# Performance work log

Measured on AMD Instinct MI355X. Metric: run time of the kernel, lower is better.

## Reference

```python
import jax, jax.numpy as jnp
import numpy as np
from jax import lax

B, N, C_IN, C_OUT = 8, 8192, 64, 128
NUM_SAMPLES, K = 2048, 32
EPS = 1e-5


def _bn(x, g, b, m, v):
    # inference-mode BatchNorm1d over channel axis 1; x: [G, C, L]
    scale = g / jnp.sqrt(v + EPS)
    return (x - m[None, :, None]) * scale[None, :, None] + b[None, :, None]


def _conv1x1(x, w):
    # kernel_size=1 Conv1d (no bias); x: [G, Cin, L], w: [Cout, Cin]
    return jnp.einsum('gck,oc->gok', x, w)


def _res_block(x, w1, g1, b1, m1, v1, w2, g2, b2, m2, v2):
    # conv-bn-relu -> conv-bn, residual add, relu (residual_factor=1.0)
    y = jax.nn.relu(_bn(_conv1x1(x, w1), g1, b1, m1, v1))
    y = _bn(_conv1x1(y, w2), g2, b2, m2, v2)
    return jax.nn.relu(y + x)


def _fps(xyz, num_samples):
    # farthest point sampling; xyz: [B,N,3] -> indices [B,S]
    b, n, _ = xyz.shape

    def step(carry, _):
        dists, last_idx = carry
        last_pt = jnp.take_along_axis(xyz, last_idx[:, None, None], axis=1)  # [B,1,3]
        d = jnp.sum((xyz - last_pt) ** 2, axis=-1)  # [B,N]
        dists = jnp.minimum(dists, d)
        nxt = jnp.argmax(dists, axis=-1).astype(jnp.int32)
        return (dists, nxt), last_idx

    init = (jnp.full((b, n), 1e10, xyz.dtype), jnp.zeros((b,), jnp.int32))
    _, idxs = lax.scan(step, init, None, length=num_samples)
    return jnp.transpose(idxs)  # [B,S]


def setup_inputs():
    key = jax.random.key(0)
    ks = jax.random.split(key, 40)
    xyz = jax.random.uniform(ks[0], (B, N, 3), jnp.float32)
    feat = jax.random.normal(ks[1], (B, N, C_IN), jnp.float32)

    def conv_w(k, o, c):
        return jax.random.normal(k, (o, c), jnp.float32) * (1.0 / np.sqrt(c).astype(np.float32))

    def bn_params(k, c):
        k1, k2, k3, k4 = jax.random.split(k, 4)
        return (1.0 + 0.1 * jax.random.normal(k1, (c,), jnp.float32),
                0.1 * jax.random.normal(k2, (c,), jnp.float32),
                0.1 * jax.random.normal(k3, (c,), jnp.float32),
                jax.random.uniform(k4, (c,), jnp.float32, 0.5, 1.5))

    inp = {'xyz': xyz, 'feat': feat}
    inp['te_w'] = conv_w(ks[2], C_OUT, 2 * C_IN)
    inp['te_g'], inp['te_b'], inp['te_m'], inp['te_v'] = bn_params(ks[3], C_OUT)
    for name, base in (('pre', 4), ('pos', 14)):
        inp[name + '_w1'] = jnp.stack([conv_w(ks[base + i], C_OUT, C_OUT) for i in range(2)])
        inp[name + '_w2'] = jnp.stack([conv_w(ks[base + 2 + i], C_OUT, C_OUT) for i in range(2)])
        bn1 = [bn_params(ks[base + 4 + i], C_OUT) for i in range(2)]
        bn2 = [bn_params(ks[base + 6 + i], C_OUT) for i in range(2)]
        for j, s in enumerate(('g', 'b', 'm', 'v')):
            inp[f'{name}_{s}1'] = jnp.stack([bn1[i][j] for i in range(2)])
            inp[f'{name}_{s}2'] = jnp.stack([bn2[i][j] for i in range(2)])
    return inp


def reference(xyz, feat, te_w, te_g, te_b, te_m, te_v,
              pre_w1, pre_w2, pre_g1, pre_b1, pre_m1, pre_v1, pre_g2, pre_b2, pre_m2, pre_v2,
              pos_w1, pos_w2, pos_g1, pos_b1, pos_m1, pos_v1, pos_g2, pos_b2, pos_m2, pos_v2):
    bsz = xyz.shape[0]
    # --- LocalGrouper: FPS centers + kNN grouping + concat center feat ---
    fps_idx = _fps(xyz, NUM_SAMPLES)                                    # [B,S]
    new_xyz = jnp.take_along_axis(xyz, fps_idx[..., None], axis=1)      # [B,S,3]
    ctr_feat = jnp.take_along_axis(feat, fps_idx[..., None], axis=1)    # [B,S,C]
    d2 = jnp.sum((new_xyz[:, :, None, :] - xyz[:, None, :, :]) ** 2, axis=-1)  # [B,S,N]
    _, knn_idx = lax.top_k(-d2, K)                                      # [B,S,K]
    grouped = feat[jnp.arange(bsz)[:, None, None], knn_idx]             # [B,S,K,C]
    ctr = jnp.broadcast_to(ctr_feat[:, :, None, :], grouped.shape)
    nf = jnp.concatenate([grouped, ctr], axis=-1)                       # [B,S,K,2C]
    # --- permute/view -> [B*S, 2C, K] ---
    x = nf.transpose(0, 1, 3, 2).reshape(bsz * NUM_SAMPLES, 2 * C_IN, K)
    x = jax.nn.relu(_bn(_conv1x1(x, te_w), te_g, te_b, te_m, te_v))     # [G,OUT,K]
    for i in range(2):
        x = _res_block(x, pre_w1[i], pre_g1[i], pre_b1[i], pre_m1[i], pre_v1[i],
                       pre_w2[i], pre_g2[i], pre_b2[i], pre_m2[i], pre_v2[i])
    x = jnp.max(x, axis=-1)                                             # adaptive_max_pool1d(.,1)
    x = x.reshape(bsz, NUM_SAMPLES, C_OUT).transpose(0, 2, 1)           # [B,OUT,S]
    for i in range(2):
        x = _res_block(x, pos_w1[i], pos_g1[i], pos_b1[i], pos_m1[i], pos_v1[i],
                       pos_w2[i], pos_g2[i], pos_b2[i], pos_m2[i], pos_v2[i])
    return new_xyz, x
```

## Files before the change

### kernel.cpp

```cpp
#include <hip/hip_runtime.h>

typedef unsigned short u16;
typedef unsigned int   u32;
typedef unsigned long long u64;

#define B_    8
#define N_    8192
#define CIN   64
#define COUT  128
#define NS    2048
#define K_    32
#define LDSPAD 136

typedef __attribute__((ext_vector_type(8))) short short8;
typedef __attribute__((ext_vector_type(4))) float f32x4;
typedef __attribute__((ext_vector_type(2))) float f32x2;

#define MFMA16(a,b,c) __builtin_amdgcn_mfma_f32_16x16x32_bf16(a,b,c,0,0,0)

__device__ __forceinline__ u16 f2bf(float f){
  u32 u = __float_as_uint(f);
  return (u16)((u + 0x7FFFu + ((u >> 16) & 1u)) >> 16);
}
__device__ __forceinline__ float bf2f(u16 h){ u32 u = ((u32)h) << 16; return __uint_as_float(u); }
__device__ __forceinline__ u32 pack2bf(float lo, float hi){ return (u32)f2bf(lo) | ((u32)f2bf(hi) << 16); }

__global__ void wcvt_kernel(const float* __restrict__ s, u16* __restrict__ d, int n){
  int i = blockIdx.x * 256 + threadIdx.x;
  if (i < n) d[i] = f2bf(s[i]);
}

__global__ void clear_kernel(int* __restrict__ fps_idx, u32* __restrict__ done){
  int i = blockIdx.x * 256 + threadIdx.x;
  if (i < B_*NS){ fps_idx[i] = -1; done[i] = 0u; }
}

struct BnPtrs { const float* g[9]; const float* b[9]; const float* m[9]; const float* v[9]; };

__global__ void bn_pre_kernel(BnPtrs p, float* __restrict__ bns){
  int set = blockIdx.x, c = threadIdx.x;
  float sc = p.g[set][c] / sqrtf(p.v[set][c] + 1e-5f);
  bns[set*256 + c]       = sc;
  bns[set*256 + 128 + c] = p.b[set][c] - p.m[set][c] * sc;
}

struct ShFps {
  __align__(16) u64  keyA[2][8];
  __align__(16) f32x4 cA[2][8];
};
struct ShMid {
  __align__(16) u16 X[8][32*LDSPAD];
  __align__(16) float scr[8][128];
};
struct ShPos {
  __align__(16) u16 X[8][32*LDSPAD];
};
union ShAll { ShFps f; ShMid m; ShPos p; char pad[83968]; };

__device__ __forceinline__ void lds_barrier(){
  __builtin_amdgcn_sched_barrier(0);
  asm volatile("s_waitcnt lgkmcnt(0)\n\ts_barrier" ::: "memory");
  __builtin_amdgcn_sched_barrier(0);
}

#define DPP_UMAX(x, ctrl) { \
  u32 o = (u32)__builtin_amdgcn_update_dpp((int)(x), (int)(x), ctrl, 0xf, 0xf, false); \
  x = (o > x) ? o : x; }

__device__ __forceinline__ u32 wave_umax63(u32 x){
  DPP_UMAX(x, 0x111)
  DPP_UMAX(x, 0x112)
  DPP_UMAX(x, 0x114)
  DPP_UMAX(x, 0x118)
  DPP_UMAX(x, 0x142)
  DPP_UMAX(x, 0x143)
  return (u32)__builtin_amdgcn_readlane((int)x, 63);
}

#define FPS_PAIR(m) { \
  f32x2 dx = PXr##m - lx2; \
  f32x2 dy = PYr##m - ly2; \
  f32x2 dz = PZr##m - lz2; \
  f32x2 t0 = dx*dx; \
  f32x2 t1 = dy*dy; \
  f32x2 t2 = dz*dz; \
  f32x2 dd = (t0 + t1) + t2; \
  f32x2 nd; \
  nd.x = fminf(Dr##m.x, dd.x); \
  nd.y = fminf(Dr##m.y, dd.y); \
  Dr##m = nd; \
  fmA = fmaxf(fmA, nd.x); \
  fmB = fmaxf(fmB, nd.y); }

#define FPS_SELK(m) { \
  if (Dr##m.y == wmf){ kk = 2*m + 1; wx = PXr##m.y; wy = PYr##m.y; wz = PZr##m.y; } \
  if (Dr##m.x == wmf){ kk = 2*m;     wx = PXr##m.x; wy = PYr##m.x; wz = PZr##m.x; } }

__device__ __forceinline__ void selmax(u64& ka, f32x4& ca, u64 kb, f32x4 cb){
  bool c = kb > ka;
  ka = c ? kb : ka;
  ca = c ? cb : ca;
}

__device__ void fps_path(const float* __restrict__ xyz, int* __restrict__ fps_idx,
                         ShFps& S, int b, int t){
  #pragma clang fp contract(off)
  const int lane = t & 63, wv = t >> 6;
  const float* xb = xyz + (size_t)b * N_ * 3;
  const int base = t * 16;
  f32x4 raw0, raw1, raw2, raw3, raw4, raw5, raw6, raw7, raw8, raw9, rawA, rawB;
  {
    const f32x4* xv = (const f32x4*)(xb + (size_t)base * 3);
    raw0 = xv[0]; raw1 = xv[1]; raw2 = xv[2];  raw3 = xv[3];
    raw4 = xv[4]; raw5 = xv[5]; raw6 = xv[6];  raw7 = xv[7];
    raw8 = xv[8]; raw9 = xv[9]; rawA = xv[10]; rawB = xv[11];
  }
  f32x2 PXr0,PXr1,PXr2,PXr3,PXr4,PXr5,PXr6,PXr7;
  f32x2 PYr0,PYr1,PYr2,PYr3,PYr4,PYr5,PYr6,PYr7;
  f32x2 PZr0,PZr1,PZr2,PZr3,PZr4,PZr5,PZr6,PZr7;
  #define GETF(k) (k<4?raw0[(k)&3]:k<8?raw1[(k)&3]:k<12?raw2[(k)&3]:k<16?raw3[(k)&3]: \
                   k<20?raw4[(k)&3]:k<24?raw5[(k)&3]:k<28?raw6[(k)&3]:k<32?raw7[(k)&3]: \
                   k<36?raw8[(k)&3]:k<40?raw9[(k)&3]:k<44?rawA[(k)&3]:rawB[(k)&3])
  #define SETP(m) { \
    PXr##m.x = GETF(6*m+0); PXr##m.y = GETF(6*m+3); \
    PYr##m.x = GETF(6*m+1); PYr##m.y = GETF(6*m+4); \
    PZr##m.x = GETF(6*m+2); PZr##m.y = GETF(6*m+5); }
  SETP(0) SETP(1) SETP(2) SETP(3) SETP(4) SETP(5) SETP(6) SETP(7)
  #undef SETP
  #undef GETF
  if (t == 0)
    __hip_atomic_store(fps_idx + b*NS, 0, __ATOMIC_RELAXED, __HIP_MEMORY_SCOPE_AGENT);
  f32x2 Dr0,Dr1,Dr2,Dr3,Dr4,Dr5,Dr6,Dr7;
  Dr0=Dr1=Dr2=Dr3=Dr4=Dr5=Dr6=Dr7=(f32x2){1e10f,1e10f};
  const float sx = xb[0], sy = xb[1], sz = xb[2];
  f32x2 lx2 = {sx,sx}, ly2 = {sy,sy}, lz2 = {sz,sz};
  int my_pi = 0;
  for (int s = 0; s < NS - 1; ++s){
    float fmA = 0.f, fmB = 0.f;
    FPS_PAIR(0) FPS_PAIR(1) FPS_PAIR(2) FPS_PAIR(3)
    FPS_PAIR(4) FPS_PAIR(5) FPS_PAIR(6) FPS_PAIR(7)
    const float fm = fmaxf(fmA, fmB);
    const u32 tbm = __float_as_uint(fm);
    const u32 wmax = wave_umax63(tbm);
    const u64 mask = __ballot(tbm == wmax);
    const int fl = __ffsll((long long)mask) - 1;
    const int sl = s & 1;
    if (lane == fl){
      const float wmf = __uint_as_float(wmax);
      int kk = 0;
      float wx = PXr0.x, wy = PYr0.x, wz = PZr0.x;
      FPS_SELK(7) FPS_SELK(6) FPS_SELK(5) FPS_SELK(4)
      FPS_SELK(3) FPS_SELK(2) FPS_SELK(1) FPS_SELK(0)
      const int pi = base + kk;
      S.keyA[sl][wv] = ((u64)wmax << 13) | (u64)(8191 - pi);
      f32x4 c; c[0] = wx; c[1] = wy; c[2] = wz; c[3] = 0.f;
      S.cA[sl][wv] = c;
    }
    lds_barrier();
    u64 k0 = S.keyA[sl][0], k1 = S.keyA[sl][1], k2 = S.keyA[sl][2], k3 = S.keyA[sl][3];
    u64 k4 = S.keyA[sl][4], k5 = S.keyA[sl][5], k6 = S.keyA[sl][6], k7 = S.keyA[sl][7];
    f32x4 c0 = S.cA[sl][0], c1 = S.cA[sl][1], c2 = S.cA[sl][2], c3 = S.cA[sl][3];
    f32x4 c4 = S.cA[sl][4], c5 = S.cA[sl][5], c6 = S.cA[sl][6], c7 = S.cA[sl][7];
    selmax(k0,c0,k1,c1); selmax(k2,c2,k3,c3); selmax(k4,c4,k5,c5); selmax(k6,c6,k7,c7);
    selmax(k0,c0,k2,c2); selmax(k4,c4,k6,c6);
    selmax(k0,c0,k4,c4);
    lx2.x = c0[0]; lx2.y = c0[0];
    ly2.x = c0[1]; ly2.y = c0[1];
    lz2.x = c0[2]; lz2.y = c0[2];
    const int pi_out = 8191 - (int)(k0 & 0x1FFFull);
    if (lane == (s & 15)) my_pi = pi_out;
    if ((s & 15) == 15 && t < 16)
      __hip_atomic_store(fps_idx + b*NS + s - 14 + t, my_pi,
                         __ATOMIC_RELAXED, __HIP_MEMORY_SCOPE_AGENT);
  }
  if (t < 15)
    __hip_atomic_store(fps_idx + b*NS + (NS - 15) + t, my_pi,
                       __ATOMIC_RELAXED, __HIP_MEMORY_SCOPE_AGENT);
}

__device__ __forceinline__ void zero_acc(f32x4 acc[8][2]){
  #pragma unroll
  for (int mt = 0; mt < 8; ++mt)
    #pragma unroll
    for (int nt = 0; nt < 2; ++nt){
      acc[mt][nt][0] = 0.f; acc[mt][nt][1] = 0.f; acc[mt][nt][2] = 0.f; acc[mt][nt][3] = 0.f;
    }
}

__device__ __forceinline__ void conv_step(const u16* __restrict__ W, const u16* __restrict__ Xw,
                                          int q, int l15, f32x4 acc[8][2]){
  #pragma unroll
  for (int kk = 0; kk < 4; ++kk){
    short8 b0 = *(const short8*)(Xw + l15*LDSPAD + kk*32 + q*8);
    short8 b1 = *(const short8*)(Xw + (16 + l15)*LDSPAD + kk*32 + q*8);
    #pragma unroll
    for (int mt = 0; mt < 8; ++mt){
      short8 a = *(const short8*)(W + (size_t)(mt*16 + l15)*COUT + kk*32 + q*8);
      acc[mt][0] = MFMA16(a, b0, acc[mt][0]);
      acc[mt][1] = MFMA16(a, b1, acc[mt][1]);
    }
  }
}

__device__ __forceinline__ void res_block(const u16* __restrict__ W1, const u16* __restrict__ W2,
    const float* __restrict__ bn1, const float* __restrict__ bn2,
    u16* __restrict__ Xw, int q, int l15, u32 resid[8][2][2], f32x4 acc[8][2], bool writeback){
  zero_acc(acc);
  conv_step(W1, Xw, q, l15, acc);
  #pragma unroll
  for (int mt = 0; mt < 8; ++mt){
    f32x4 sc = *(const f32x4*)(bn1 + mt*16 + q*4);
    f32x4 bi = *(const f32x4*)(bn1 + 128 + mt*16 + q*4);
    #pragma unroll
    for (int nt = 0; nt < 2; ++nt){
      float y0 = fmaxf(fmaf(acc[mt][nt][0], sc[0], bi[0]), 0.f);
      float y1 = fmaxf(fmaf(acc[mt][nt][1], sc[1], bi[1]), 0.f);
      float y2 = fmaxf(fmaf(acc[mt][nt][2], sc[2], bi[2]), 0.f);
      float y3 = fmaxf(fmaf(acc[mt][nt][3], sc[3], bi[3]), 0.f);
      *(uint2*)(Xw + (nt*16 + l15)*LDSPAD + mt*16 + q*4) = make_uint2(pack2bf(y0,y1), pack2bf(y2,y3));
    }
  }
  __syncthreads();
  zero_acc(acc);
  conv_step(W2, Xw, q, l15, acc);
  #pragma unroll
  for (int mt = 0; mt < 8; ++mt){
    f32x4 sc = *(const f32x4*)(bn2 + mt*16 + q*4);
    f32x4 bi = *(const f32x4*)(bn2 + 128 + mt*16 + q*4);
    #pragma unroll
    for (int nt = 0; nt < 2; ++nt){
      float r0 = bf2f((u16)(resid[mt][nt][0] & 0xFFFFu));
      float r1 = bf2f((u16)(resid[mt][nt][0] >> 16));
      float r2 = bf2f((u16)(resid[mt][nt][1] & 0xFFFFu));
      float r3 = bf2f((u16)(resid[mt][nt][1] >> 16));
      float y0 = fmaxf(fmaf(acc[mt][nt][0], sc[0], bi[0]) + r0, 0.f);
      float y1 = fmaxf(fmaf(acc[mt][nt][1], sc[1], bi[1]) + r1, 0.f);
      float y2 = fmaxf(fmaf(acc[mt][nt][2], sc[2], bi[2]) + r2, 0.f);
      float y3 = fmaxf(fmaf(acc[mt][nt][3], sc[3], bi[3]) + r3, 0.f);
      acc[mt][nt][0] = y0; acc[mt][nt][1] = y1; acc[mt][nt][2] = y2; acc[mt][nt][3] = y3;
      if (writeback){
        u32 p0 = pack2bf(y0,y1), p1 = pack2bf(y2,y3);
        resid[mt][nt][0] = p0; resid[mt][nt][1] = p1;
        *(uint2*)(Xw + (nt*16 + l15)*LDSPAD + mt*16 + q*4) = make_uint2(p0, p1);
      }
    }
  }
  if (writeback) __syncthreads();
}

__device__ void knnmid_path(const float* __restrict__ xyz, const float* __restrict__ feat,
    const u16* __restrict__ te_w, const u16* __restrict__ pre_w1, const u16* __restrict__ pre_w2,
    const float* __restrict__ bns, int* __restrict__ fps_idx,
    u16* __restrict__ x_mid, u32* __restrict__ done, float* __restrict__ out_xyz,
    u16* __restrict__ Xw, float* __restrict__ scrw, int g, int lane){
  #pragma clang fp contract(off)
  const int b = g >> 11;
  const float* xb = xyz + (size_t)b * N_ * 3;

  int raw;
  for (;;){
    raw = __hip_atomic_load(fps_idx + g, __ATOMIC_RELAXED, __HIP_MEMORY_SCOPE_AGENT);
    if (raw >= 0) break;
    __builtin_amdgcn_s_sleep(2);
  }
  const int ci = raw & (N_ - 1);
  const float cx = xb[ci*3], cy = xb[ci*3+1], cz = xb[ci*3+2];
  if (lane < 3) out_xyz[g*3 + lane] = xb[ci*3 + lane];

  float rd = __uint_as_float(0x7F800000u); int ri = 0x7FFFFFFF;
  float r31d = rd; int r31i = ri;
  for (int c = 0; c < N_/64; ++c){
    const int pid = c*64 + lane;
    float dx = xb[pid*3]   - cx;
    float dy = xb[pid*3+1] - cy;
    float dz = xb[pid*3+2] - cz;
    float t0 = dx*dx, t1 = dy*dy, t2 = dz*dz;
    float d2 = (t0 + t1) + t2;
    u64 m = __ballot((d2 < r31d) || (d2 == r31d && pid < r31i));
    while (m){
      int l = __ffsll((long long)m) - 1; m &= m - 1;
      float v = __shfl(d2, l); int vi = c*64 + l;
      if (!((v < r31d) || (v == r31d && vi < r31i))) continue;
      bool lt = (rd < v) || (rd == v && ri < vi);
      int pos = __popcll(__ballot(lt));
      float prd = __shfl_up(rd, 1); int pri = __shfl_up(ri, 1);
      if (lane == pos){ rd = v; ri = vi; }
      else if (lane > pos){ rd = prd; ri = pri; }
      r31d = __shfl(rd, 31); r31i = __shfl(ri, 31);
    }
  }

  const int q = lane >> 4, l15 = lane & 15;
  const float* fb = feat + (size_t)b * N_ * CIN;
  #pragma unroll
  for (int it = 0; it < 4; ++it){
    int lidx = it*64 + lane;
    int kq = lidx & 7;
    int col = it*8 + (lane >> 3);
    int nb = __shfl(ri, col) & (N_ - 1);
    f32x4 a0 = *(const f32x4*)(fb + (size_t)nb*CIN + kq*8);
    f32x4 a1 = *(const f32x4*)(fb + (size_t)nb*CIN + kq*8 + 4);
    *(uint2*)(Xw + col*LDSPAD + kq*8)     = make_uint2(pack2bf(a0[0],a0[1]), pack2bf(a0[2],a0[3]));
    *(uint2*)(Xw + col*LDSPAD + kq*8 + 4) = make_uint2(pack2bf(a1[0],a1[1]), pack2bf(a1[2],a1[3]));
    f32x4 c0 = *(const f32x4*)(fb + (size_t)ci*CIN + kq*8);
    f32x4 c1 = *(const f32x4*)(fb + (size_t)ci*CIN + kq*8 + 4);
    *(uint2*)(Xw + col*LDSPAD + 64 + kq*8)     = make_uint2(pack2bf(c0[0],c0[1]), pack2bf(c0[2],c0[3]));
    *(uint2*)(Xw + col*LDSPAD + 64 + kq*8 + 4) = make_uint2(pack2bf(c1[0],c1[1]), pack2bf(c1[2],c1[3]));
  }
  __syncthreads();

  f32x4 acc[8][2];
  u32 resid[8][2][2];
  zero_acc(acc);
  conv_step(te_w, Xw, q, l15, acc);
  #pragma unroll
  for (int mt = 0; mt < 8; ++mt){
    f32x4 sc = *(const f32x4*)(bns + mt*16 + q*4);
    f32x4 bi = *(const f32x4*)(bns + 128 + mt*16 + q*4);
    #pragma unroll
    for (int nt = 0; nt < 2; ++nt){
      float y0 = fmaxf(fmaf(acc[mt][nt][0], sc[0], bi[0]), 0.f);
      float y1 = fmaxf(fmaf(acc[mt][nt][1], sc[1], bi[1]), 0.f);
      float y2 = fmaxf(fmaf(acc[mt][nt][2], sc[2], bi[2]), 0.f);
      float y3 = fmaxf(fmaf(acc[mt][nt][3], sc[3], bi[3]), 0.f);
      u32 p0 = pack2bf(y0,y1), p1 = pack2bf(y2,y3);
      resid[mt][nt][0] = p0; resid[mt][nt][1] = p1;
      *(uint2*)(Xw + (nt*16 + l15)*LDSPAD + mt*16 + q*4) = make_uint2(p0, p1);
    }
  }
  __syncthreads();

  res_block(pre_w1,             pre_w2,             bns + 256, bns + 512,  Xw, q, l15, resid, acc, true);
  res_block(pre_w1 + COUT*COUT, pre_w2 + COUT*COUT, bns + 768, bns + 1024, Xw, q, l15, resid, acc, false);

  float mx[8][4];
  #pragma unroll
  for (int mt = 0; mt < 8; ++mt)
    #pragma unroll
    for (int r = 0; r < 4; ++r){
      float m0 = fmaxf(acc[mt][0][r], acc[mt][1][r]);
      #pragma unroll
      for (int off = 1; off < 16; off <<= 1) m0 = fmaxf(m0, __shfl_xor(m0, off));
      mx[mt][r] = m0;
    }
  if (l15 == 0){
    #pragma unroll
    for (int mt = 0; mt < 8; ++mt){
      f32x4 vv; vv[0] = mx[mt][0]; vv[1] = mx[mt][1]; vv[2] = mx[mt][2]; vv[3] = mx[mt][3];
      *(f32x4*)(scrw + mt*16 + q*4) = vv;
    }
  }
  __syncthreads();
  float v0 = scrw[lane*2], v1 = scrw[lane*2 + 1];
  *(u32*)(x_mid + (size_t)g*COUT + lane*2) = pack2bf(v0, v1);
  if (lane == 0)
    __hip_atomic_store(done + g, 1u, __ATOMIC_RELEASE, __HIP_MEMORY_SCOPE_AGENT);
}

__device__ void pos_path(const u16* __restrict__ x_mid,
    const u16* __restrict__ pos_w1, const u16* __restrict__ pos_w2,
    const float* __restrict__ bns, float* __restrict__ out_x,
    u32* __restrict__ done, u16* __restrict__ Xw, int g, int lane){
  const int q = lane >> 4, l15 = lane & 15;
  const int gc0 = g * 32;
  const int b = gc0 >> 11, s0 = gc0 & 2047;
  for (;;){
    u32 d = (lane < 32)
      ? __hip_atomic_load(done + gc0 + lane, __ATOMIC_RELAXED, __HIP_MEMORY_SCOPE_AGENT)
      : 1u;
    if (__all(d != 0)) break;
    __builtin_amdgcn_s_sleep(16);
  }
  __builtin_amdgcn_fence(__ATOMIC_ACQUIRE, "agent");
  #pragma unroll
  for (int it = 0; it < 8; ++it){
    int lidx = it*64 + lane;
    int col = lidx >> 4, kq = lidx & 15;
    uint4 v = *(const uint4*)(x_mid + (size_t)(gc0 + col)*COUT + kq*8);
    *(uint4*)(Xw + col*LDSPAD + kq*8) = v;
  }
  __syncthreads();
  u32 resid[8][2][2];
  #pragma unroll
  for (int mt = 0; mt < 8; ++mt)
    #pragma unroll
    for (int nt = 0; nt < 2; ++nt){
      uint2 rr = *(const uint2*)(Xw + (nt*16 + l15)*LDSPAD + mt*16 + q*4);
      resid[mt][nt][0] = rr.x; resid[mt][nt][1] = rr.y;
    }
  f32x4 acc[8][2];
  res_block(pos_w1,             pos_w2,             bns + 1280, bns + 1536, Xw, q, l15, resid, acc, true);
  res_block(pos_w1 + COUT*COUT, pos_w2 + COUT*COUT, bns + 1792, bns + 2048, Xw, q, l15, resid, acc, false);
  #pragma unroll
  for (int mt = 0; mt < 8; ++mt)
    #pragma unroll
    for (int nt = 0; nt < 2; ++nt)
      #pragma unroll
      for (int r = 0; r < 4; ++r){
        int row = mt*16 + q*4 + r;
        int colx = s0 + nt*16 + l15;
        out_x[(size_t)(b*COUT + row)*NS + colx] = acc[mt][nt][r];
      }
}

#define GRID_FPS    B_
#define GRID_KM     (B_*NS/8)
#define GRID_POS    (B_*NS/K_/8)

__global__ __launch_bounds__(512) void mega_kernel(
    const float* __restrict__ xyz, const float* __restrict__ feat,
    const u16* __restrict__ te_w, const u16* __restrict__ pre_w1, const u16* __restrict__ pre_w2,
    const u16* __restrict__ pos_w1, const u16* __restrict__ pos_w2,
    const float* __restrict__ bns, int* __restrict__ fps_idx,
    u16* __restrict__ x_mid, u32* __restrict__ done,
    float* __restrict__ out_xyz, float* __restrict__ out_x){
  __shared__ ShAll sh;
  const int bid = blockIdx.x;
  const int t = threadIdx.x;
  const int wid = t >> 6, lane = t & 63;
  if (bid < GRID_FPS){
    fps_path(xyz, fps_idx, sh.f, bid, t);
  } else if (bid < GRID_FPS + GRID_KM){
    const int i = bid - GRID_FPS;
    const int g0 = (i & 7) * NS + (i >> 3) * 8;
    if (t == 0){
      while (__hip_atomic_load(fps_idx + g0 + 7, __ATOMIC_RELAXED,
                               __HIP_MEMORY_SCOPE_AGENT) < 0)
        __builtin_amdgcn_s_sleep(16);
    }
    __syncthreads();
    knnmid_path(xyz, feat, te_w, pre_w1, pre_w2, bns, fps_idx, x_mid, done, out_xyz,
                sh.m.X[wid], sh.m.scr[wid], g0 + wid, lane);
  } else {
    const int idx = (bid - GRID_FPS - GRID_KM)*8 + wid;
    const int g = (idx & 7) * (NS/K_) + (idx >> 3);
    pos_path(x_mid, pos_w1, pos_w2, bns, out_x, done, sh.p.X[wid], g, lane);
  }
}

extern "C" void kernel_launch(void* const* d_in, const int* in_sizes, int n_in,
                              void* d_out, int out_size, void* d_ws, size_t ws_size,
                              hipStream_t stream){
  (void)in_sizes; (void)n_in; (void)out_size; (void)ws_size;
  const float* xyz    = (const float*)d_in[0];
  const float* feat   = (const float*)d_in[1];

  char* ws = (char*)d_ws;
  float* bns     = (float*)ws;
  u16*   wbf     = (u16*)(ws + 16384);
  int*   fps_idx = (int*)(ws + 16384 + 294912);
  u32*   done    = (u32*)(ws + 16384 + 294912 + 65536);
  u16*   x_mid   = (u16*)(ws + 16384 + 294912 + 65536 + 65536);
  float* out_xyz = (float*)d_out;
  float* out_x   = (float*)d_out + B_*NS*3;

  u16* te_w   = wbf;
  u16* pre_w1 = wbf + 16384;
  u16* pre_w2 = wbf + 49152;
  u16* pos_w1 = wbf + 81920;
  u16* pos_w2 = wbf + 114688;
  wcvt_kernel<<<64,  256, 0, stream>>>((const float*)d_in[2],  te_w,   16384);
  wcvt_kernel<<<128, 256, 0, stream>>>((const float*)d_in[7],  pre_w1, 32768);
  wcvt_kernel<<<128, 256, 0, stream>>>((const float*)d_in[8],  pre_w2, 32768);
  wcvt_kernel<<<128, 256, 0, stream>>>((const float*)d_in[17], pos_w1, 32768);
  wcvt_kernel<<<128, 256, 0, stream>>>((const float*)d_in[18], pos_w2, 32768);
  clear_kernel<<<64, 256, 0, stream>>>(fps_idx, done);

  BnPtrs bp;
  const int gi[9] = {3, 9, 10, 9, 10, 19, 20, 19, 20};
  const int bbi[9]= {4, 11,12, 11,12, 21, 22, 21, 22};
  const int mi[9] = {5, 13,14, 13,14, 23, 24, 23, 24};
  const int vi[9] = {6, 15,16, 15,16, 25, 26, 25, 26};
  const int of[9] = {0, 0, 0, 128,128, 0, 0, 128,128};
  for (int k = 0; k < 9; ++k){
    bp.g[k] = (const float*)d_in[gi[k]]  + of[k];
    bp.b[k] = (const float*)d_in[bbi[k]] + of[k];
    bp.m[k] = (const float*)d_in[mi[k]]  + of[k];
    bp.v[k] = (const float*)d_in[vi[k]]  + of[k];
  }

  bn_pre_kernel<<<9, 128, 0, stream>>>(bp, bns);
  mega_kernel<<<GRID_FPS + GRID_KM + GRID_POS, 512, 0, stream>>>(
      xyz, feat, te_w, pre_w1, pre_w2, pos_w1, pos_w2, bns,
      fps_idx, x_mid, done, out_xyz, out_x);
}
```

Measured before the change: 2.812 ms.

## Fold weight/BN prep into mega kernel and use LDS atomicMax for FPS reduction

Removes the separate weight-conversion and BN-precompute launches and performs them in one extra block of the mega kernel, with a release flag that the kNN blocks poll before starting. Separately, the per-step FPS cross-wave argmax is replaced by a 64-bit atomicMax on a triple-buffered LDS slot, so each thread reads a single winner key instead of eight keys plus a select tree. This aims to cut launch overhead and shorten the serial FPS step, at the cost of LDS atomic contention and a new inter-block dependency on the prep block.

```diff
diff --git a/kernel.cpp b/kernel.cpp
--- a/kernel.cpp
+++ b/kernel.cpp
@@ -25,27 +25,17 @@
 __device__ __forceinline__ float bf2f(u16 h){ u32 u = ((u32)h) << 16; return __uint_as_float(u); }
 __device__ __forceinline__ u32 pack2bf(float lo, float hi){ return (u32)f2bf(lo) | ((u32)f2bf(hi) << 16); }
 
-__global__ void wcvt_kernel(const float* __restrict__ s, u16* __restrict__ d, int n){
-  int i = blockIdx.x * 256 + threadIdx.x;
-  if (i < n) d[i] = f2bf(s[i]);
-}
-
-__global__ void clear_kernel(int* __restrict__ fps_idx, u32* __restrict__ done){
+__global__ void clear_kernel(int* __restrict__ fps_idx, u32* __restrict__ done,
+                             u32* __restrict__ wready){
   int i = blockIdx.x * 256 + threadIdx.x;
   if (i < B_*NS){ fps_idx[i] = -1; done[i] = 0u; }
+  if (i == 0) wready[0] = 0u;
 }
 
 struct BnPtrs { const float* g[9]; const float* b[9]; const float* m[9]; const float* v[9]; };
 
-__global__ void bn_pre_kernel(BnPtrs p, float* __restrict__ bns){
-  int set = blockIdx.x, c = threadIdx.x;
-  float sc = p.g[set][c] / sqrtf(p.v[set][c] + 1e-5f);
-  bns[set*256 + c]       = sc;
-  bns[set*256 + 128 + c] = p.b[set][c] - p.m[set][c] * sc;
-}
-
 struct ShFps {
-  __align__(16) u64  keyA[2][8];
+  u64 key3[3];
   __align__(16) f32x4 cA[2][8];
 };
 struct ShMid {
@@ -96,12 +86,6 @@
   if (Dr##m.y == wmf){ kk = 2*m + 1; wx = PXr##m.y; wy = PYr##m.y; wz = PZr##m.y; } \
   if (Dr##m.x == wmf){ kk = 2*m;     wx = PXr##m.x; wy = PYr##m.x; wz = PZr##m.x; } }
 
-__device__ __forceinline__ void selmax(u64& ka, f32x4& ca, u64 kb, f32x4 cb){
-  bool c = kb > ka;
-  ka = c ? kb : ka;
-  ca = c ? cb : ca;
-}
-
 __device__ void fps_path(const float* __restrict__ xyz, int* __restrict__ fps_idx,
                          ShFps& S, int b, int t){
   #pragma clang fp contract(off)
@@ -128,13 +112,17 @@
   SETP(0) SETP(1) SETP(2) SETP(3) SETP(4) SETP(5) SETP(6) SETP(7)
   #undef SETP
   #undef GETF
-  if (t == 0)
+  if (t == 0){
+    S.key3[0] = 0; S.key3[1] = 0; S.key3[2] = 0;
     __hip_atomic_store(fps_idx + b*NS, 0, __ATOMIC_RELAXED, __HIP_MEMORY_SCOPE_AGENT);
+  }
   f32x2 Dr0,Dr1,Dr2,Dr3,Dr4,Dr5,Dr6,Dr7;
   Dr0=Dr1=Dr2=Dr3=Dr4=Dr5=Dr6=Dr7=(f32x2){1e10f,1e10f};
   const float sx = xb[0], sy = xb[1], sz = xb[2];
   f32x2 lx2 = {sx,sx}, ly2 = {sy,sy}, lz2 = {sz,sz};
+  __syncthreads();
   int my_pi = 0;
+  int sl3 = 0, zsl = 1;
   for (int s = 0; s < NS - 1; ++s){
     float fmA = 0.f, fmB = 0.f;
     FPS_PAIR(0) FPS_PAIR(1) FPS_PAIR(2) FPS_PAIR(3)
@@ -152,30 +140,56 @@
       FPS_SELK(7) FPS_SELK(6) FPS_SELK(5) FPS_SELK(4)
       FPS_SELK(3) FPS_SELK(2) FPS_SELK(1) FPS_SELK(0)
       const int pi = base + kk;
-      S.keyA[sl][wv] = ((u64)wmax << 13) | (u64)(8191 - pi);
+      atomicMax((unsigned long long*)&S.key3[sl3],
+                ((u64)wmax << 13) | (u64)(8191 - pi));
       f32x4 c; c[0] = wx; c[1] = wy; c[2] = wz; c[3] = 0.f;
       S.cA[sl][wv] = c;
     }
+    if (t == 0) S.key3[zsl] = 0;
     lds_barrier();
-    u64 k0 = S.keyA[sl][0], k1 = S.keyA[sl][1], k2 = S.keyA[sl][2], k3 = S.keyA[sl][3];
-    u64 k4 = S.keyA[sl][4], k5 = S.keyA[sl][5], k6 = S.keyA[sl][6], k7 = S.keyA[sl][7];
-    f32x4 c0 = S.cA[sl][0], c1 = S.cA[sl][1], c2 = S.cA[sl][2], c3 = S.cA[sl][3];
-    f32x4 c4 = S.cA[sl][4], c5 = S.cA[sl][5], c6 = S.cA[sl][6], c7 = S.cA[sl][7];
-    selmax(k0,c0,k1,c1); selmax(k2,c2,k3,c3); selmax(k4,c4,k5,c5); selmax(k6,c6,k7,c7);
-    selmax(k0,c0,k2,c2); selmax(k4,c4,k6,c6);
-    selmax(k0,c0,k4,c4);
+    const u64 win = S.key3[sl3];
+    const int pi_out = 8191 - (int)(win & 0x1FFFull);
+    const f32x4 c0 = S.cA[sl][pi_out >> 10];
     lx2.x = c0[0]; lx2.y = c0[0];
     ly2.x = c0[1]; ly2.y = c0[1];
     lz2.x = c0[2]; lz2.y = c0[2];
-    const int pi_out = 8191 - (int)(k0 & 0x1FFFull);
     if (lane == (s & 15)) my_pi = pi_out;
     if ((s & 15) == 15 && t < 16)
       __hip_atomic_store(fps_idx + b*NS + s - 14 + t, my_pi,
                          __ATOMIC_RELAXED, __HIP_MEMORY_SCOPE_AGENT);
+    sl3 = zsl; zsl = (zsl == 2) ? 0 : (zsl + 1);
   }
   if (t < 15)
     __hip_atomic_store(fps_idx + b*NS + (NS - 15) + t, my_pi,
                        __ATOMIC_RELAXED, __HIP_MEMORY_SCOPE_AGENT);
+}
+
+__device__ __forceinline__ void st_wt(u32* p, u32 v){
+  __hip_atomic_store(p, v, __ATOMIC_RELAXED, __HIP_MEMORY_SCOPE_AGENT);
+}
+
+__device__ void prep_path(const float* s_te, const float* s_pre1, const float* s_pre2,
+    const float* s_pos1, const float* s_pos2,
+    u16* te_w, u16* pre_w1, u16* pre_w2, u16* pos_w1, u16* pos_w2,
+    BnPtrs bp, float* bns, u32* wready, int t){
+  #define CVT2(src, dst, n) \
+    for (int i = t; i < (n)/2; i += 512) \
+      st_wt((u32*)(dst) + i, pack2bf((src)[2*i], (src)[2*i+1]));
+  CVT2(s_te,   te_w,   16384)
+  CVT2(s_pre1, pre_w1, 32768)
+  CVT2(s_pre2, pre_w2, 32768)
+  CVT2(s_pos1, pos_w1, 32768)
+  CVT2(s_pos2, pos_w2, 32768)
+  #undef CVT2
+  for (int i = t; i < 9*128; i += 512){
+    int set = i >> 7, c = i & 127;
+    float sc = bp.g[set][c] / sqrtf(bp.v[set][c] + 1e-5f);
+    st_wt((u32*)(bns + set*256 + c),       __float_as_uint(sc));
+    st_wt((u32*)(bns + set*256 + 128 + c), __float_as_uint(bp.b[set][c] - bp.m[set][c] * sc));
+  }
+  __syncthreads();
+  if (t == 0)
+    __hip_atomic_store(wready, 1u, __ATOMIC_RELEASE, __HIP_MEMORY_SCOPE_AGENT);
 }
 
 __device__ __forceinline__ void zero_acc(f32x4 acc[8][2]){
@@ -404,15 +418,19 @@
 }
 
 #define GRID_FPS    B_
+#define GRID_PREP   1
 #define GRID_KM     (B_*NS/8)
 #define GRID_POS    (B_*NS/K_/8)
 
 __global__ __launch_bounds__(512) void mega_kernel(
     const float* __restrict__ xyz, const float* __restrict__ feat,
-    const u16* __restrict__ te_w, const u16* __restrict__ pre_w1, const u16* __restrict__ pre_w2,
-    const u16* __restrict__ pos_w1, const u16* __restrict__ pos_w2,
-    const float* __restrict__ bns, int* __restrict__ fps_idx,
-    u16* __restrict__ x_mid, u32* __restrict__ done,
+    const float* __restrict__ s_te, const float* __restrict__ s_pre1,
+    const float* __restrict__ s_pre2, const float* __restrict__ s_pos1,
+    const float* __restrict__ s_pos2, BnPtrs bp,
+    u16* __restrict__ te_w, u16* __restrict__ pre_w1, u16* __restrict__ pre_w2,
+    u16* __restrict__ pos_w1, u16* __restrict__ pos_w2,
+    float* __restrict__ bns, int* __restrict__ fps_idx,
+    u16* __restrict__ x_mid, u32* __restrict__ done, u32* __restrict__ wready,
     float* __restrict__ out_xyz, float* __restrict__ out_x){
   __shared__ ShAll sh;
   const int bid = blockIdx.x;
@@ -420,11 +438,15 @@
   const int wid = t >> 6, lane = t & 63;
   if (bid < GRID_FPS){
     fps_path(xyz, fps_idx, sh.f, bid, t);
-  } else if (bid < GRID_FPS + GRID_KM){
-    const int i = bid - GRID_FPS;
+  } else if (bid < GRID_FPS + GRID_PREP){
+    prep_path(s_te, s_pre1, s_pre2, s_pos1, s_pos2,
+              te_w, pre_w1, pre_w2, pos_w1, pos_w2, bp, bns, wready, t);
+  } else if (bid < GRID_FPS + GRID_PREP + GRID_KM){
+    const int i = bid - GRID_FPS - GRID_PREP;
     const int g0 = (i & 7) * NS + (i >> 3) * 8;
     if (t == 0){
-      while (__hip_atomic_load(fps_idx + g0 + 7, __ATOMIC_RELAXED,
+      while (__hip_atomic_load(wready, __ATOMIC_RELAXED, __HIP_MEMORY_SCOPE_AGENT) == 0u ||
+             __hip_atomic_load(fps_idx + g0 + 7, __ATOMIC_RELAXED,
                                __HIP_MEMORY_SCOPE_AGENT) < 0)
         __builtin_amdgcn_s_sleep(16);
     }
@@ -432,7 +454,7 @@
     knnmid_path(xyz, feat, te_w, pre_w1, pre_w2, bns, fps_idx, x_mid, done, out_xyz,
                 sh.m.X[wid], sh.m.scr[wid], g0 + wid, lane);
   } else {
-    const int idx = (bid - GRID_FPS - GRID_KM)*8 + wid;
+    const int idx = (bid - GRID_FPS - GRID_PREP - GRID_KM)*8 + wid;
     const int g = (idx & 7) * (NS/K_) + (idx >> 3);
     pos_path(x_mid, pos_w1, pos_w2, bns, out_x, done, sh.p.X[wid], g, lane);
   }
@@ -447,6 +469,7 @@
 
   char* ws = (char*)d_ws;
   float* bns     = (float*)ws;
+  u32*   wready  = (u32*)(ws + 12288);
   u16*   wbf     = (u16*)(ws + 16384);
   int*   fps_idx = (int*)(ws + 16384 + 294912);
   u32*   done    = (u32*)(ws + 16384 + 294912 + 65536);
@@ -459,12 +482,6 @@
   u16* pre_w2 = wbf + 49152;
   u16* pos_w1 = wbf + 81920;
   u16* pos_w2 = wbf + 114688;
-  wcvt_kernel<<<64,  256, 0, stream>>>((const float*)d_in[2],  te_w,   16384);
-  wcvt_kernel<<<128, 256, 0, stream>>>((const float*)d_in[7],  pre_w1, 32768);
-  wcvt_kernel<<<128, 256, 0, stream>>>((const float*)d_in[8],  pre_w2, 32768);
-  wcvt_kernel<<<128, 256, 0, stream>>>((const float*)d_in[17], pos_w1, 32768);
-  wcvt_kernel<<<128, 256, 0, stream>>>((const float*)d_in[18], pos_w2, 32768);
-  clear_kernel<<<64, 256, 0, stream>>>(fps_idx, done);
 
   BnPtrs bp;
   const int gi[9] = {3, 9, 10, 9, 10, 19, 20, 19, 20};
@@ -479,8 +496,11 @@
     bp.v[k] = (const float*)d_in[vi[k]]  + of[k];
   }
 
-  bn_pre_kernel<<<9, 128, 0, stream>>>(bp, bns);
-  mega_kernel<<<GRID_FPS + GRID_KM + GRID_POS, 512, 0, stream>>>(
-      xyz, feat, te_w, pre_w1, pre_w2, pos_w1, pos_w2, bns,
-      fps_idx, x_mid, done, out_xyz, out_x);
-}
+  clear_kernel<<<64, 256, 0, stream>>>(fps_idx, done, wready);
+  mega_kernel<<<GRID_FPS + GRID_PREP + GRID_KM + GRID_POS, 512, 0, stream>>>(
+      xyz, feat,
+      (const float*)d_in[2], (const float*)d_in[7], (const float*)d_in[8],
+      (const float*)d_in[17], (const float*)d_in[18], bp,
+      te_w, pre_w1, pre_w2, pos_w1, pos_w2,
+      bns, fps_idx, x_mid, done, wready, out_xyz, out_x);
+}
```

Result: no change. 2.827 ms (+0.5%).
